# Kernel optimization log

Hardware: AMD Instinct MI355X
Metric: run time of the kernel (lower is better)

Reference implementation:

```python
import jax, jax.numpy as jnp
import numpy as np

B, M, A, F = 8, 512, 16, 128  # batch, atoms/messages, irrep dim (n_ang_mom**2=16), feature channels
CG_DENSITY = 0.25             # CG coefficient tensors are highly sparse; emulate with a random mask


def setup_inputs() -> dict:
    key = jax.random.key(0)
    kx, ky, kc, km = jax.random.split(key, 4)
    x = jax.random.normal(kx, (B, M, A, F), dtype=jnp.float32)
    y = jax.random.normal(ky, (B, M, A, F), dtype=jnp.float32)
    # stand-in for cgc_multiplier(n_ang_mom): sparse [a, d, c] Clebsch-Gordan coefficient tensor
    cgc_dense = jax.random.normal(kc, (A, A, A), dtype=jnp.float32)
    mask = jax.random.bernoulli(km, CG_DENSITY, (A, A, A))
    cgc = jnp.where(mask, cgc_dense, 0.0)
    return {"x": x, "y": y, "cgc": cgc}


def reference(x, y, cgc):
    # TensorProductContractionLayer.call: triple contraction over irrep indices a, c
    # x: [b,m,a,f], y: [b,m,c,f], cgc: [a,d,c] -> res: [b,m,d,f]
    return jnp.einsum('bmaf,bmcf,adc->bmdf', x, y, cgc)
```

## Files before the change

### kernel.cpp

```cpp
#include <hip/hip_runtime.h>


typedef __attribute__((ext_vector_type(2))) _Float16 half2v;
typedef __attribute__((ext_vector_type(8))) _Float16 half8;
typedef __attribute__((ext_vector_type(4))) float    floatx4;

#define AA 16
#define FF 128
#define BM_PER_BLOCK 8
#define NBUF 3

union H8 { half2v h2[4]; half8 h8; };

static __device__ __forceinline__ half2v pkrtz(float a, float b) {
    return __builtin_bit_cast(half2v, __builtin_amdgcn_cvt_pkrtz(a, b));
}

static __device__ __forceinline__ void gload_lds16(const float* g, float* l) {
    __builtin_amdgcn_global_load_lds(
        (const __attribute__((address_space(1))) void*)g,
        (__attribute__((address_space(3))) void*)l,
        16, 0, 0);
}

#define WAITB(N) do {                                            \
    asm volatile("s_waitcnt vmcnt(" #N ")" ::: "memory");        \
    __builtin_amdgcn_sched_barrier(0);                           \
    __builtin_amdgcn_s_barrier();                                \
    __builtin_amdgcn_sched_barrier(0);                           \
} while (0)

__global__ __launch_bounds__(256, 2)
void tpc_mfma_vmcnt_kernel(const float* __restrict__ x,
                           const float* __restrict__ y,
                           const float* __restrict__ cgc,
                           float* __restrict__ out) {
    __shared__ float lx[NBUF][AA * FF];
    __shared__ float ly[NBUF][AA * FF];

    const int tid  = threadIdx.x;
    const int w    = tid >> 6;
    const int lane = tid & 63;
    const int L    = lane & 15;
    const int quad = lane >> 4;
    const int qh   = quad >> 1;
    const int c0   = (quad & 1) * 8;

    const int bm0 = blockIdx.x * BM_PER_BLOCK;
    const size_t stride = (size_t)(AA * FF);
    const int off = w * 512 + lane * 4;
    const int f0  = w * 32 + L;

    auto STAGE = [&](int i) {
        const float* xb = x + (size_t)(bm0 + i) * stride;
        const float* yb = y + (size_t)(bm0 + i) * stride;
        float* lxd = &lx[i % NBUF][0];
        float* lyd = &ly[i % NBUF][0];
        gload_lds16(xb + off,       lxd + off);
        gload_lds16(xb + off + 256, lxd + off + 256);
        gload_lds16(yb + off,       lyd + off);
        gload_lds16(yb + off + 256, lyd + off + 256);
    };

    STAGE(0);
    STAGE(1);

    half8 wfrag[8];
#pragma unroll
    for (int t = 0; t < 8; ++t) {
        const float* wp = cgc + (2 * t + qh) * (AA * AA) + L * AA + c0;
        const floatx4 w0 = *(const floatx4*)(wp);
        const floatx4 w1 = *(const floatx4*)(wp + 4);
        H8 wa;
        wa.h2[0] = pkrtz(w0.x, w0.y);
        wa.h2[1] = pkrtz(w0.z, w0.w);
        wa.h2[2] = pkrtz(w1.x, w1.y);
        wa.h2[3] = pkrtz(w1.z, w1.w);
        wfrag[t] = wa.h8;
    }

    auto COMPUTE = [&](int i) {
        const float* lxc = &lx[i % NBUF][0];
        const float* lyc = &ly[i % NBUF][0];

        float xvA[8], xvB[8], yvA[8], yvB[8];
#pragma unroll
        for (int j = 0; j < 8; ++j) {
            yvA[j] = lyc[(c0 + j) * FF + f0];
            yvB[j] = lyc[(c0 + j) * FF + f0 + 16];
        }
#pragma unroll
        for (int t = 0; t < 8; ++t) {
            xvA[t] = lxc[(2 * t + qh) * FF + f0];
            xvB[t] = lxc[(2 * t + qh) * FF + f0 + 16];
        }

        half2v ypA[4], ypB[4];
#pragma unroll
        for (int jj = 0; jj < 4; ++jj) {
            ypA[jj] = pkrtz(yvA[2 * jj], yvA[2 * jj + 1]);
            ypB[jj] = pkrtz(yvB[2 * jj], yvB[2 * jj + 1]);
        }

        floatx4 acc0 = {0.f, 0.f, 0.f, 0.f};
        floatx4 acc1 = {0.f, 0.f, 0.f, 0.f};
#pragma unroll
        for (int t = 0; t < 8; ++t) {
            half2v xp = pkrtz(xvA[t], xvA[t]);
            H8 b0;
            b0.h2[0] = xp * ypA[0];
            b0.h2[1] = xp * ypA[1];
            b0.h2[2] = xp * ypA[2];
            b0.h2[3] = xp * ypA[3];
            acc0 = __builtin_amdgcn_mfma_f32_16x16x32_f16(wfrag[t], b0.h8, acc0, 0, 0, 0);

            xp = pkrtz(xvB[t], xvB[t]);
            H8 b1;
            b1.h2[0] = xp * ypB[0];
            b1.h2[1] = xp * ypB[1];
            b1.h2[2] = xp * ypB[2];
            b1.h2[3] = xp * ypB[3];
            acc1 = __builtin_amdgcn_mfma_f32_16x16x32_f16(wfrag[t], b1.h8, acc1, 0, 0, 0);
        }

        float* ob = out + (size_t)(bm0 + i) * stride;
#pragma unroll
        for (int r = 0; r < 4; ++r) {
            const int row = (quad * 4 + r) * FF;
            ob[row + f0]      = acc0[r];
            ob[row + f0 + 16] = acc1[r];
        }
    };

#define BODY(i, N) do { WAITB(N); COMPUTE(i); if ((i) + 2 < BM_PER_BLOCK) STAGE((i) + 2); } while (0)
    BODY(0, 4);
    BODY(1, 12);
    BODY(2, 12);
    BODY(3, 12);
    BODY(4, 12);
    BODY(5, 12);
    BODY(6, 12);
    BODY(7, 8);
#undef BODY
}

extern "C" void kernel_launch(void* const* d_in, const int* in_sizes, int n_in,
                              void* d_out, int out_size, void* d_ws, size_t ws_size,
                              hipStream_t stream) {
    const float* x   = (const float*)d_in[0];
    const float* y   = (const float*)d_in[1];
    const float* cgc = (const float*)d_in[2];
    float* out = (float*)d_out;

    hipLaunchKernelGGL(tpc_mfma_vmcnt_kernel, dim3(512), dim3(256), 0, stream,
                       x, y, cgc, out);
}
```

Measured before the change: 106.4 us.

## Halve rows per block, double-buffer LDS, and raise occupancy to four blocks

Each block now processes 4 batch-message rows instead of 8, so the grid doubles to 1024 blocks. The LDS ring shrinks from three buffers to two with a one-ahead prefetch, and the next stage is issued right after the barrier, before compute. Launch bounds now ask for 4 blocks per CU, and the sched_barriers around the wait are dropped. The aim is more resident waves and blocks to hide memory latency, at the cost of a shallower prefetch and per-block cgc fragment setup repeated twice as often.

```diff
diff --git a/kernel.cpp b/kernel.cpp
--- a/kernel.cpp
+++ b/kernel.cpp
@@ -7,8 +7,7 @@
 
 #define AA 16
 #define FF 128
-#define BM_PER_BLOCK 8
-#define NBUF 3
+#define BM_PER_BLOCK 4
 
 union H8 { half2v h2[4]; half8 h8; };
 
@@ -25,18 +24,16 @@
 
 #define WAITB(N) do {                                            \
     asm volatile("s_waitcnt vmcnt(" #N ")" ::: "memory");        \
-    __builtin_amdgcn_sched_barrier(0);                           \
     __builtin_amdgcn_s_barrier();                                \
-    __builtin_amdgcn_sched_barrier(0);                           \
 } while (0)
 
-__global__ __launch_bounds__(256, 2)
-void tpc_mfma_vmcnt_kernel(const float* __restrict__ x,
-                           const float* __restrict__ y,
-                           const float* __restrict__ cgc,
-                           float* __restrict__ out) {
-    __shared__ float lx[NBUF][AA * FF];
-    __shared__ float ly[NBUF][AA * FF];
+__global__ __launch_bounds__(256, 4)
+void tpc_mfma_cnt_kernel(const float* __restrict__ x,
+                         const float* __restrict__ y,
+                         const float* __restrict__ cgc,
+                         float* __restrict__ out) {
+    __shared__ float lx[2][AA * FF];
+    __shared__ float ly[2][AA * FF];
 
     const int tid  = threadIdx.x;
     const int w    = tid >> 6;
@@ -54,8 +51,8 @@
     auto STAGE = [&](int i) {
         const float* xb = x + (size_t)(bm0 + i) * stride;
         const float* yb = y + (size_t)(bm0 + i) * stride;
-        float* lxd = &lx[i % NBUF][0];
-        float* lyd = &ly[i % NBUF][0];
+        float* lxd = &lx[i & 1][0];
+        float* lyd = &ly[i & 1][0];
         gload_lds16(xb + off,       lxd + off);
         gload_lds16(xb + off + 256, lxd + off + 256);
         gload_lds16(yb + off,       lyd + off);
@@ -63,7 +60,6 @@
     };
 
     STAGE(0);
-    STAGE(1);
 
     half8 wfrag[8];
 #pragma unroll
@@ -80,8 +76,8 @@
     }
 
     auto COMPUTE = [&](int i) {
-        const float* lxc = &lx[i % NBUF][0];
-        const float* lyc = &ly[i % NBUF][0];
+        const float* lxc = &lx[i & 1][0];
+        const float* lyc = &ly[i & 1][0];
 
         float xvA[8], xvB[8], yvA[8], yvB[8];
 #pragma unroll
@@ -132,16 +128,10 @@
         }
     };
 
-#define BODY(i, N) do { WAITB(N); COMPUTE(i); if ((i) + 2 < BM_PER_BLOCK) STAGE((i) + 2); } while (0)
-    BODY(0, 4);
-    BODY(1, 12);
-    BODY(2, 12);
-    BODY(3, 12);
-    BODY(4, 12);
-    BODY(5, 12);
-    BODY(6, 12);
-    BODY(7, 8);
-#undef BODY
+    WAITB(0); STAGE(1); COMPUTE(0);
+    WAITB(8); STAGE(2); COMPUTE(1);
+    WAITB(8); STAGE(3); COMPUTE(2);
+    WAITB(8);           COMPUTE(3);
 }
 
 extern "C" void kernel_launch(void* const* d_in, const int* in_sizes, int n_in,
@@ -152,6 +142,6 @@
     const float* cgc = (const float*)d_in[2];
     float* out = (float*)d_out;
 
-    hipLaunchKernelGGL(tpc_mfma_vmcnt_kernel, dim3(512), dim3(256), 0, stream,
+    hipLaunchKernelGGL(tpc_mfma_cnt_kernel, dim3(1024), dim3(256), 0, stream,
                        x, y, cgc, out);
 }
```

Measured after the change: 107.2 us. Within noise of the previous version (+0.8%).
